# Performance work log

Measured on AMD Instinct MI355X. Metric: run time of the kernel, lower is better.

Reference implementation:

```python
import jax, jax.numpy as jnp
import numpy as np

D, S, L, W, H, V = 64, 64, 64, 300, 300, 50000
NEG = jnp.float32(-9999999.0)


def setup_inputs() -> dict:
    key = jax.random.key(0)
    ks = jax.random.split(key, 16)
    n = lambda k, shape, s=0.05: jax.random.normal(k, shape, dtype=jnp.float32) * s
    return {
        "word_indices": jax.random.randint(ks[0], (D, S, L), 0, V),
        "E": n(ks[1], (V, W), 0.1),
        "W_sent": n(ks[2], (H, W)), "b_sent": jnp.zeros((H,), jnp.float32),
        "W_par": n(ks[3], (H, H)), "b_par": jnp.zeros((H,), jnp.float32),
        "W_ch": n(ks[4], (H, H)), "b_ch": jnp.zeros((H,), jnp.float32),
        "w_root": n(ks[5], (H,)), "b_root": jnp.zeros((), jnp.float32),
        "root_embed": n(ks[6], (H,)),
        "W_r": n(ks[7], (H, 3 * H)), "b_r": jnp.zeros((H,), jnp.float32),
        "W_cls": n(ks[8], (2, H)), "b_cls": jnp.zeros((2,), jnp.float32),
    }


def reference(word_indices, E, W_sent, b_sent, W_par, b_par, W_ch, b_ch,
              w_root, b_root, root_embed, W_r, b_r, W_cls, b_cls):
    lrelu = lambda x: jax.nn.leaky_relu(x, 0.01)
    # Ragged pad+gather stage of the original, dense here (all lengths == L)
    word_embed = E[word_indices]                 # [D,S,L,W]
    # 0.5*(X[l-1] + reverse(reverse(X))[l-1]) == X[l-1]; LSTM outputs unused in source
    x_last = word_embed[:, :, -1, :]             # [D,S,W]
    enc = lrelu(x_last @ W_sent.T + b_sent)      # [D,S,H] sentence encodings
    # Pairwise parent-child edge scores (O(S^2) dots in the original loops)
    P = lrelu(enc @ W_par.T + b_par)             # [D,S,H]
    C = lrelu(enc @ W_ch.T + b_ch)               # [D,S,H]
    A = jnp.einsum('dih,djh->dij', P, C)         # [D,S,S]
    A = jnp.where(jnp.eye(S, dtype=bool)[None], NEG, A)
    A = jax.nn.softmax(A, axis=1)                # Softmax(dim=0) per doc: over parents i
    scores = enc @ w_root + b_root               # [D,S] root scores
    fri = jax.nn.softmax(scores, axis=1)         # Softmax(dim=0) over sentences
    # ri[i] = r_embeds([enc_i, sum_k A[k,i]*enc_k + fri_i*root, enc_i*sum_k A[i,k]])
    tmp = jnp.einsum('dki,dkh->dih', A, enc)     # [D,S,H]
    agg = tmp + fri[..., None] * root_embed      # [D,S,H]
    tmp3 = enc * A.sum(axis=2, keepdims=True)    # [D,S,H]
    ri = lrelu(jnp.concatenate([enc, agg, tmp3], axis=-1) @ W_r.T + b_r)  # [D,S,H]
    final = ri.mean(axis=1)                      # [D,H]
    out = final @ W_cls.T + b_cls                # [D,2]
    return out, A, fri
```

## Files before the change

### kernel.cpp

```cpp
#include <hip/hip_runtime.h>

#define NEG_INF (-9999999.0f)

typedef __attribute__((ext_vector_type(8))) short bf16x8;
typedef __attribute__((ext_vector_type(4))) float f32x4;
typedef unsigned short us;
typedef unsigned int u32;

#define MFMA16 __builtin_amdgcn_mfma_f32_16x16x32_bf16

__device__ __forceinline__ float b2f(us u) {
  union { unsigned int i; float f; } x; x.i = ((unsigned int)u) << 16; return x.f;
}
__device__ __forceinline__ us f2b(float f) {
  union { float f; unsigned int i; } x; x.f = f;
  unsigned int r = x.i + 0x7fffu + ((x.i >> 16) & 1u);
  return (us)(r >> 16);
}
__device__ __forceinline__ float lrelu(float v) { return v > 0.f ? v : 0.01f * v; }
__device__ __forceinline__ bf16x8 ld8(const us* p) { return *reinterpret_cast<const bf16x8*>(p); }
__device__ __forceinline__ int swz(int row) { return (row & 7) << 4; }

__global__ __launch_bounds__(256) void k_prep(
    const float* __restrict__ Ws, const float* __restrict__ Wp, const float* __restrict__ Wc,
    const float* __restrict__ Wr, const float* __restrict__ root,
    us* __restrict__ Wsb, us* __restrict__ Wpb, us* __restrict__ Wcb,
    us* __restrict__ Wr3b, float* __restrict__ c2) {
  int task = blockIdx.y;
  int gid = blockIdx.x * 256 + threadIdx.x;
  const int stride = 240 * 256;
  if (task < 3) {
    const float* src = (task == 0) ? Ws : (task == 1) ? Wp : Wc;
    us* dst = (task == 0) ? Wsb : (task == 1) ? Wpb : Wcb;
    for (int i = gid; i < 320 * 320; i += stride) {
      int r = i / 320, c = i - r * 320;
      dst[i] = (r < 300 && c < 300) ? f2b(src[r * 300 + c]) : (us)0;
    }
  } else if (task == 3) {
    for (int i = gid; i < 3 * 320 * 320; i += stride) {
      int seg = i / 102400, rem = i - seg * 102400;
      int r = rem / 320, c = rem - r * 320;
      Wr3b[i] = (r < 300 && c < 300) ? f2b(Wr[r * 900 + seg * 300 + c]) : (us)0;
    }
  } else {
    for (int i = gid; i < 320 * 8; i += stride) {
      int c = i >> 3, p = i & 7;
      float s = 0.f;
      if (c < 300)
        for (int h = p; h < 300; h += 8) s = fmaf(Wr[c * 900 + 300 + h], root[h], s);
      s += __shfl_xor(s, 1); s += __shfl_xor(s, 2); s += __shfl_xor(s, 4);
      if (p == 0) c2[c] = s;
    }
  }
}

template<int M, int NT, int KS>
__device__ __forceinline__ void sweepM(const us* __restrict__ Alds, const int (&rr)[M],
    int q, int lo, const us* __restrict__ Bg, int n0, f32x4 (&acc)[M][NT]) {
  const char* ab = (const char*)Alds;
  int ao[M], sw[M];
#pragma unroll
  for (int m = 0; m < M; ++m) { ao[m] = rr[m] * 640; sw[m] = swz(rr[m]); }
  const us* br[NT];
#pragma unroll
  for (int t = 0; t < NT; ++t)
    br[t] = Bg + (long)((n0 + t) * 16 + lo) * 320 + 8 * q;
  bf16x8 aC[M], aN[M], b0[NT], b1[NT];
#pragma unroll
  for (int m = 0; m < M; ++m) {
    aC[m] = *(const bf16x8*)(ab + ao[m] + ((16 * q) ^ sw[m]));
    aN[m] = *(const bf16x8*)(ab + ao[m] + ((64 + 16 * q) ^ sw[m]));
  }
#pragma unroll
  for (int t = 0; t < NT; ++t) b0[t] = ld8(br[t]);
#pragma unroll
  for (int t = 0; t < NT; ++t) b1[t] = ld8(br[t] + 32);
#pragma unroll
  for (int ks = 0; ks < KS - 2; ++ks) {
    bf16x8 aF[M], bF[NT];
    const int kb = 64 * (ks + 2) + 16 * q;
#pragma unroll
    for (int m = 0; m < M; ++m) aF[m] = *(const bf16x8*)(ab + ao[m] + (kb ^ sw[m]));
#pragma unroll
    for (int t = 0; t < NT; ++t) bF[t] = ld8(br[t] + (ks + 2) * 32);
#pragma unroll
    for (int t = 0; t < NT; ++t)
#pragma unroll
      for (int m = 0; m < M; ++m)
        acc[m][t] = MFMA16(aC[m], b0[t], acc[m][t], 0, 0, 0);
#pragma unroll
    for (int m = 0; m < M; ++m) { aC[m] = aN[m]; aN[m] = aF[m]; }
#pragma unroll
    for (int t = 0; t < NT; ++t) { b0[t] = b1[t]; b1[t] = bF[t]; }
  }
#pragma unroll
  for (int t = 0; t < NT; ++t)
#pragma unroll
    for (int m = 0; m < M; ++m) acc[m][t] = MFMA16(aC[m], b0[t], acc[m][t], 0, 0, 0);
#pragma unroll
  for (int t = 0; t < NT; ++t)
#pragma unroll
    for (int m = 0; m < M; ++m) acc[m][t] = MFMA16(aN[m], b1[t], acc[m][t], 0, 0, 0);
}

template<int NT, int KS>
__device__ __forceinline__ void sweepT(const us* __restrict__ es, int q, int lo,
    const us* __restrict__ Ag, int n0, f32x4 (&acc)[NT]) {
  const char* eb = (const char*)es;
  const int bo = lo * 640, sb = swz(lo);
  const us* ar[NT];
#pragma unroll
  for (int t = 0; t < NT; ++t)
    ar[t] = Ag + (long)((n0 + t) * 16 + lo) * 320 + 8 * q;
  bf16x8 a0[NT], a1[NT];
#pragma unroll
  for (int t = 0; t < NT; ++t) a0[t] = ld8(ar[t]);
  bf16x8 b0 = *(const bf16x8*)(eb + bo + ((16 * q) ^ sb));
#pragma unroll
  for (int t = 0; t < NT; ++t) a1[t] = ld8(ar[t] + 32);
  bf16x8 b1 = *(const bf16x8*)(eb + bo + ((64 + 16 * q) ^ sb));
#pragma unroll
  for (int ks = 0; ks < KS - 2; ++ks) {
    bf16x8 a2[NT];
#pragma unroll
    for (int t = 0; t < NT; ++t) a2[t] = ld8(ar[t] + (ks + 2) * 32);
    bf16x8 b2 = *(const bf16x8*)(eb + bo + ((64 * (ks + 2) + 16 * q) ^ sb));
#pragma unroll
    for (int t = 0; t < NT; ++t) acc[t] = MFMA16(a0[t], b0, acc[t], 0, 0, 0);
#pragma unroll
    for (int t = 0; t < NT; ++t) { a0[t] = a1[t]; a1[t] = a2[t]; }
    b0 = b1; b1 = b2;
  }
#pragma unroll
  for (int t = 0; t < NT; ++t) acc[t] = MFMA16(a0[t], b0, acc[t], 0, 0, 0);
#pragma unroll
  for (int t = 0; t < NT; ++t) acc[t] = MFMA16(a1[t], b1, acc[t], 0, 0, 0);
}

template<int NT>
__device__ __forceinline__ void sweepG(const us* __restrict__ Ab,
    const us* __restrict__ Bb, int m0, int nt0, int lo, int q, int ksn, f32x4* acc) {
  const us* ar = Ab + (long)(m0 + lo) * 320 + 8 * q;
  const us* br[NT];
#pragma unroll
  for (int t = 0; t < NT; ++t)
    br[t] = Bb + (long)((nt0 + t) * 16 + lo) * 320 + 8 * q;
  bf16x8 a0 = ld8(ar), a1 = ld8(ar + 32);
  bf16x8 b0[NT], b1[NT];
#pragma unroll
  for (int t = 0; t < NT; ++t) b0[t] = ld8(br[t]);
#pragma unroll
  for (int t = 0; t < NT; ++t) b1[t] = ld8(br[t] + 32);
  for (int ks = 0; ks < ksn - 2; ++ks) {
    bf16x8 a2 = ld8(ar + (ks + 2) * 32);
    bf16x8 b2[NT];
#pragma unroll
    for (int t = 0; t < NT; ++t) b2[t] = ld8(br[t] + (ks + 2) * 32);
#pragma unroll
    for (int t = 0; t < NT; ++t)
      acc[t] = MFMA16(a0, b0[t], acc[t], 0, 0, 0);
    a0 = a1; a1 = a2;
#pragma unroll
    for (int t = 0; t < NT; ++t) { b0[t] = b1[t]; b1[t] = b2[t]; }
  }
#pragma unroll
  for (int t = 0; t < NT; ++t)
    acc[t] = MFMA16(a0, b0[t], acc[t], 0, 0, 0);
#pragma unroll
  for (int t = 0; t < NT; ++t)
    acc[t] = MFMA16(a1, b1[t], acc[t], 0, 0, 0);
}

__global__ __launch_bounds__(256) void k_enc(
    const int* __restrict__ wi, const float* __restrict__ E,
    const us* __restrict__ Wsb, const float* __restrict__ b_sent,
    const float* __restrict__ w_root,
    us* __restrict__ encG, float* __restrict__ scG) {
  __shared__ __align__(16) us xs[16 * 320];
  __shared__ __align__(16) us es[16 * 320];
  int t = threadIdx.x;
  int r0g = blockIdx.x * 16;
  {
    int row = t >> 4, p = t & 15;
    int widx = wi[((r0g + row) << 6) + 63];
    const float4* er = (const float4*)(E + (long)widx * 300);
    char* rowb = (char*)xs + row * 640;
    int sw = swz(row);
    for (int j = p; j < 75; j += 16) {
      float4 v = er[j];
      *(ushort4*)(rowb + ((8 * j) ^ sw)) =
          make_ushort4(f2b(v.x), f2b(v.y), f2b(v.z), f2b(v.w));
    }
    for (int c = 300 + p; c < 320; c += 16)
      *(us*)(rowb + ((2 * c) ^ sw)) = 0;
  }
  __syncthreads();
  int w = t >> 6, lane = t & 63, lo = lane & 15, q = lane >> 4;
  const f32x4 z4 = {0.f, 0.f, 0.f, 0.f};
  int rr[1] = { lo };
  f32x4 acc[1][5];
#pragma unroll
  for (int b = 0; b < 5; ++b) acc[0][b] = z4;
  sweepM<1, 5, 10>(xs, rr, q, lo, Wsb, w * 5, acc);
#pragma unroll
  for (int tt = 0; tt < 5; ++tt) {
    int col = (w * 5 + tt) * 16 + lo;
    float bb = (col < 300) ? b_sent[col] : 0.f;
#pragma unroll
    for (int r = 0; r < 4; ++r) {
      int row = 4 * q + r;
      us hv = (col < 300) ? f2b(lrelu(acc[0][tt][r] + bb)) : (us)0;
      *(us*)((char*)es + row * 640 + ((2 * col) ^ swz(row))) = hv;
      encG[(long)(r0g + row) * 320 + col] = hv;
    }
  }
  __syncthreads();
  {
    int row = t >> 4, p = t & 15;
    float s = 0.f;
    for (int cch = p; cch < 38; cch += 16) {
      bf16x8 v = *(const bf16x8*)((const char*)es + row * 640 + ((16 * cch) ^ swz(row)));
#pragma unroll
      for (int e = 0; e < 8; ++e) {
        int h = cch * 8 + e;
        if (h < 300) s = fmaf(b2f((us)v[e]), w_root[h], s);
      }
    }
    s += __shfl_xor(s, 1); s += __shfl_xor(s, 2); s += __shfl_xor(s, 4); s += __shfl_xor(s, 8);
    if (p == 0) scG[r0g + row] = s;
  }
}

__global__ __launch_bounds__(256) void k_panels(
    const us* __restrict__ encG,
    const us* __restrict__ Wpb, const us* __restrict__ Wcb, const us* __restrict__ Wrb,
    const float* __restrict__ b_par, const float* __restrict__ b_ch,
    us* __restrict__ Pg, us* __restrict__ Cg, us* __restrict__ G1g, us* __restrict__ G3g,
    us* __restrict__ G2eT) {
  __shared__ __align__(16) us es[16 * 320];
  int t = threadIdx.x, task = blockIdx.y, rt = blockIdx.x;
  {
    const float4* src = (const float4*)(encG + (long)rt * 16 * 320);
    for (int i = t; i < 640; i += 256) {
      int row = i / 40, c16 = i - row * 40;
      float4 v = src[i];
      *(float4*)((char*)es + row * 640 + ((c16 * 16) ^ swz(row))) = v;
    }
  }
  __syncthreads();
  int w = t >> 6, lane = t & 63, lo = lane & 15, q = lane >> 4;
  const f32x4 z4 = {0.f, 0.f, 0.f, 0.f};
  if (task == 4) {
    f32x4 acc[5];
#pragma unroll
    for (int b = 0; b < 5; ++b) acc[b] = z4;
    sweepT<5, 10>(es, q, lo, Wrb + 102400, w * 5, acc);
#pragma unroll
    for (int tt = 0; tt < 5; ++tt)
#pragma unroll
      for (int r = 0; r < 4; ++r) {
        int h = (w * 5 + tt) * 16 + 4 * q + r;
        G2eT[(long)h * 4096 + rt * 16 + lo] = (h < 300) ? f2b(acc[tt][r]) : (us)0;
      }
  } else {
    const us* Bg = (task == 0) ? Wpb : (task == 1) ? Wcb : (task == 2) ? Wrb : Wrb + 204800;
    int rr[1] = { lo };
    f32x4 acc[1][5];
#pragma unroll
    for (int b = 0; b < 5; ++b) acc[0][b] = z4;
    sweepM<1, 5, 10>(es, rr, q, lo, Bg, w * 5, acc);
    if (task < 2) {
      const float* bias = (task == 0) ? b_par : b_ch;
      us* outb = (task == 0) ? Pg : Cg;
#pragma unroll
      for (int tt = 0; tt < 5; ++tt) {
        int col = (w * 5 + tt) * 16 + lo;
        float bb = (col < 300) ? bias[col] : 0.f;
#pragma unroll
        for (int r = 0; r < 4; ++r) {
          int row = rt * 16 + 4 * q + r;
          outb[(long)row * 320 + col] =
              (col < 300) ? f2b(lrelu(acc[0][tt][r] + bb)) : (us)0;
        }
      }
    } else {
      us* outb = (task == 2) ? G1g : G3g;
#pragma unroll
      for (int tt = 0; tt < 5; ++tt) {
        int col = (w * 5 + tt) * 16 + lo;
        if (col < 300)
#pragma unroll
          for (int r = 0; r < 4; ++r)
            outb[(long)(rt * 16 + 4 * q + r) * 320 + col] = f2b(acc[0][tt][r]);
      }
    }
  }
}

__global__ __launch_bounds__(512) void k_doc(
    const us* __restrict__ Pg, const us* __restrict__ Cg, const us* __restrict__ G2eT,
    const us* __restrict__ G1g, const us* __restrict__ G3g,
    const float* __restrict__ scG, const float* __restrict__ c2,
    const float* __restrict__ b_r, const float* __restrict__ W_cls,
    const float* __restrict__ b_cls,
    float* __restrict__ outp, float* __restrict__ outA, float* __restrict__ outF) {
  __shared__ __align__(16) float LA[64 * 68];
  __shared__ __align__(16) us AtL[64 * 72];
  __shared__ float pm[512], ps[512];
  __shared__ float friS[64], rsS[64];
  __shared__ float finP2[4 * 320];
  int d = blockIdx.x, t = threadIdx.x;
  int w = t >> 6, lane = t & 63, lo = lane & 15, q = lane >> 4;
  const f32x4 z4 = {0.f, 0.f, 0.f, 0.f};

  if (t < 64) {
    float sc = scG[d * 64 + t], m = sc;
#pragma unroll
    for (int o = 32; o > 0; o >>= 1) m = fmaxf(m, __shfl_xor(m, o));
    float e = expf(sc - m), sum = e;
#pragma unroll
    for (int o = 32; o > 0; o >>= 1) sum += __shfl_xor(sum, o);
    float f = e / sum;
    friS[t] = f;
    outF[d * 64 + t] = f;
  }

  {
    const us* Pd = Pg + (long)d * 64 * 320;
    const us* Cd = Cg + (long)d * 64 * 320;
    int m = w >> 1, np = (w & 1) * 2;
    f32x4 acc2[2] = { z4, z4 };
    sweepG<2>(Pd, Cd, m * 16, np, lo, q, 10, acc2);
#pragma unroll
    for (int r = 0; r < 4; ++r) {
      int row = m * 16 + 4 * q + r;
      int c0 = np * 16 + lo, c1 = c0 + 16;
      LA[row * 68 + c0] = (row == c0) ? NEG_INF : acc2[0][r];
      LA[row * 68 + c1] = (row == c1) ? NEG_INF : acc2[1][r];
    }
  }
  __syncthreads();

  {
    int j = lane;
    float mx = -3.0e38f;
#pragma unroll
    for (int ii = 0; ii < 8; ++ii) mx = fmaxf(mx, LA[(w * 8 + ii) * 68 + j]);
    pm[w * 64 + j] = mx;
    __syncthreads();
    float gm = pm[j];
#pragma unroll
    for (int k = 1; k < 8; ++k) gm = fmaxf(gm, pm[k * 64 + j]);
    float ev[8], ss = 0.f;
#pragma unroll
    for (int ii = 0; ii < 8; ++ii) {
      float e = expf(LA[(w * 8 + ii) * 68 + j] - gm);
      ev[ii] = e; ss += e;
    }
    ps[w * 64 + j] = ss;
    __syncthreads();
    float tot = ps[j];
#pragma unroll
    for (int k = 1; k < 8; ++k) tot += ps[k * 64 + j];
    float inv = 1.f / tot;
    float* Ad = outA + (long)d * 4096;
#pragma unroll
    for (int ii = 0; ii < 8; ++ii) {
      int i = w * 8 + ii;
      float a = ev[ii] * inv;
      Ad[i * 64 + j] = a;
      AtL[j * 72 + i] = f2b(a);
      LA[i * 68 + j] = a;
    }
  }
  __syncthreads();
  if (t < 64) {
    float s = 0.f;
    for (int jj = 0; jj < 64; ++jj) s += LA[t * 68 + jj];
    rsS[t] = s;
  }
  __syncthreads();

  {
    int mg = w & 3, nh = w >> 2;
    f32x4 a10[10];
#pragma unroll
    for (int b = 0; b < 10; ++b) a10[b] = z4;
#pragma unroll
    for (int ks = 0; ks < 2; ++ks) {
      bf16x8 aA = ld8(AtL + (mg * 16 + lo) * 72 + 32 * ks + 8 * q);
#pragma unroll
      for (int tt = 0; tt < 10; ++tt) {
        bf16x8 bv = ld8(G2eT + (long)((nh * 10 + tt) * 16 + lo) * 4096 +
                        d * 64 + 32 * ks + 8 * q);
        a10[tt] = MFMA16(aA, bv, a10[tt], 0, 0, 0);
      }
    }
#pragma unroll
    for (int tt = 0; tt < 10; ++tt) {
      int col = (nh * 10 + tt) * 16 + lo;
      if (col < 300) {
        float bb = b_r[col], cc = c2[col];
        float csum = 0.f;
#pragma unroll
        for (int r = 0; r < 4; ++r) {
          int i = mg * 16 + 4 * q + r;
          float g1 = b2f(G1g[(long)(d * 64 + i) * 320 + col]);
          float g3 = b2f(G3g[(long)(d * 64 + i) * 320 + col]);
          csum += lrelu(a10[tt][r] + g1 + rsS[i] * g3 + friS[i] * cc + bb);
        }
        csum += __shfl_xor(csum, 16);
        csum += __shfl_xor(csum, 32);
        if (q == 0) finP2[mg * 320 + col] = csum;
      }
    }
  }
  __syncthreads();

  if (t < 128) {
    int cls = t >> 6, ln = t & 63;
    float s = 0.f;
    for (int h = ln; h < 300; h += 64)
      s += (finP2[h] + finP2[320 + h] + finP2[640 + h] + finP2[960 + h]) *
           W_cls[cls * 300 + h];
#pragma unroll
    for (int o = 32; o > 0; o >>= 1) s += __shfl_xor(s, o);
    if (ln == 0) outp[d * 2 + cls] = s * 0.015625f + b_cls[cls];
  }
}

extern "C" void kernel_launch(void* const* d_in, const int* in_sizes, int n_in,
                              void* d_out, int out_size, void* d_ws, size_t ws_size,
                              hipStream_t stream) {
  const int*   wi     = (const int*)d_in[0];
  const float* E      = (const float*)d_in[1];
  const float* W_sent = (const float*)d_in[2];
  const float* b_sent = (const float*)d_in[3];
  const float* W_par  = (const float*)d_in[4];
  const float* b_par  = (const float*)d_in[5];
  const float* W_ch   = (const float*)d_in[6];
  const float* b_ch   = (const float*)d_in[7];
  const float* w_root = (const float*)d_in[8];
  const float* b_root = (const float*)d_in[9];  (void)b_root;
  const float* root_e = (const float*)d_in[10];
  const float* W_r    = (const float*)d_in[11];
  const float* b_r    = (const float*)d_in[12];
  const float* W_cls  = (const float*)d_in[13];
  const float* b_cls  = (const float*)d_in[14];

  us* B = (us*)d_ws;
  us* Wsb   = B;
  us* Wpb   = B + 102400;
  us* Wcb   = B + 204800;
  us* Wr3b  = B + 307200;
  float* c2 = (float*)(B + 614400);
  us* encG  = B + 615040;
  us* Pg    = B + 1925760;
  us* Cg    = B + 3236480;
  us* G1g   = B + 4547200;
  us* G3g   = B + 5857920;
  us* G2eT  = B + 7168640;
  float* scG = (float*)(B + 8479360);

  float* outp = (float*)d_out;
  float* outA = outp + 128;
  float* outF = outp + 128 + 262144;

  k_prep<<<dim3(240, 5), 256, 0, stream>>>(W_sent, W_par, W_ch, W_r, root_e,
                                           Wsb, Wpb, Wcb, Wr3b, c2);
  k_enc<<<256, 256, 0, stream>>>(wi, E, Wsb, b_sent, w_root, encG, scG);
  k_panels<<<dim3(256, 5), 256, 0, stream>>>(encG, Wpb, Wcb, Wr3b,
                                             b_par, b_ch, Pg, Cg, G1g, G3g, G2eT);
  k_doc<<<64, 512, 0, stream>>>(Pg, Cg, G2eT, G1g, G3g, scG, c2,
                                b_r, W_cls, b_cls, outp, outA, outF);
}
```

Measured before the change: 189.4 us.

## Overlap weight conversion with encoder and process 32-row tiles in panels

The single prep kernel is split in two. Only the W_sent conversion runs ahead of the encoder. The W_par, W_ch and W_r conversions and the root projection run as a second blockIdx.y slice of the encoder launch, so they overlap with the sentence encoding. The panel kernel now loads 32 encoded rows per block instead of 16 and computes two M-tiles per B-fragment load, which halves the global weight traffic per output row and halves the grid. This costs more registers and LDS per block, and with fewer blocks there is less parallelism.

```diff
diff --git a/kernel.cpp b/kernel.cpp
--- a/kernel.cpp
+++ b/kernel.cpp
@@ -21,164 +21,188 @@
 __device__ __forceinline__ bf16x8 ld8(const us* p) { return *reinterpret_cast<const bf16x8*>(p); }
 __device__ __forceinline__ int swz(int row) { return (row & 7) << 4; }
 
-__global__ __launch_bounds__(256) void k_prep(
-    const float* __restrict__ Ws, const float* __restrict__ Wp, const float* __restrict__ Wc,
+__global__ __launch_bounds__(256) void k_prep0(
+    const float* __restrict__ Ws, us* __restrict__ Wsb) {
+  int gid = blockIdx.x * 256 + threadIdx.x;
+  for (int i = gid; i < 320 * 320; i += 128 * 256) {
+    int r = i / 320, c = i - r * 320;
+    Wsb[i] = (r < 300 && c < 300) ? f2b(Ws[r * 300 + c]) : (us)0;
+  }
+}
+
+template<int M, int NT, int KS>
+__device__ __forceinline__ void sweepM(const us* __restrict__ Alds, const int (&rr)[M],
+    int q, int lo, const us* __restrict__ Bg, int n0, f32x4 (&acc)[M][NT]) {
+  const char* ab = (const char*)Alds;
+  int ao[M], sw[M];
+#pragma unroll
+  for (int m = 0; m < M; ++m) { ao[m] = rr[m] * 640; sw[m] = swz(rr[m]); }
+  const us* br[NT];
+#pragma unroll
+  for (int t = 0; t < NT; ++t)
+    br[t] = Bg + (long)((n0 + t) * 16 + lo) * 320 + 8 * q;
+  bf16x8 aC[M], aN[M], b0[NT], b1[NT];
+#pragma unroll
+  for (int m = 0; m < M; ++m) {
+    aC[m] = *(const bf16x8*)(ab + ao[m] + ((16 * q) ^ sw[m]));
+    aN[m] = *(const bf16x8*)(ab + ao[m] + ((64 + 16 * q) ^ sw[m]));
+  }
+#pragma unroll
+  for (int t = 0; t < NT; ++t) b0[t] = ld8(br[t]);
+#pragma unroll
+  for (int t = 0; t < NT; ++t) b1[t] = ld8(br[t] + 32);
+#pragma unroll
+  for (int ks = 0; ks < KS - 2; ++ks) {
+    bf16x8 aF[M], bF[NT];
+    const int kb = 64 * (ks + 2) + 16 * q;
+#pragma unroll
+    for (int m = 0; m < M; ++m) aF[m] = *(const bf16x8*)(ab + ao[m] + (kb ^ sw[m]));
+#pragma unroll
+    for (int t = 0; t < NT; ++t) bF[t] = ld8(br[t] + (ks + 2) * 32);
+#pragma unroll
+    for (int t = 0; t < NT; ++t)
+#pragma unroll
+      for (int m = 0; m < M; ++m)
+        acc[m][t] = MFMA16(aC[m], b0[t], acc[m][t], 0, 0, 0);
+#pragma unroll
+    for (int m = 0; m < M; ++m) { aC[m] = aN[m]; aN[m] = aF[m]; }
+#pragma unroll
+    for (int t = 0; t < NT; ++t) { b0[t] = b1[t]; b1[t] = bF[t]; }
+  }
+#pragma unroll
+  for (int t = 0; t < NT; ++t)
+#pragma unroll
+    for (int m = 0; m < M; ++m) acc[m][t] = MFMA16(aC[m], b0[t], acc[m][t], 0, 0, 0);
+#pragma unroll
+  for (int t = 0; t < NT; ++t)
+#pragma unroll
+    for (int m = 0; m < M; ++m) acc[m][t] = MFMA16(aN[m], b1[t], acc[m][t], 0, 0, 0);
+}
+
+template<int NT, int KS>
+__device__ __forceinline__ void sweepT2(const us* __restrict__ es, int q, int lo,
+    const us* __restrict__ Ag, int n0, f32x4 (&acc)[2][NT]) {
+  const char* eb = (const char*)es;
+  int bo[2] = { lo * 640, (lo + 16) * 640 };
+  int sb[2] = { swz(lo), swz(lo + 16) };
+  const us* ar[NT];
+#pragma unroll
+  for (int t = 0; t < NT; ++t)
+    ar[t] = Ag + (long)((n0 + t) * 16 + lo) * 320 + 8 * q;
+  bf16x8 a0[NT], a1[NT], bC[2], bN[2];
+#pragma unroll
+  for (int t = 0; t < NT; ++t) a0[t] = ld8(ar[t]);
+#pragma unroll
+  for (int h = 0; h < 2; ++h)
+    bC[h] = *(const bf16x8*)(eb + bo[h] + ((16 * q) ^ sb[h]));
+#pragma unroll
+  for (int t = 0; t < NT; ++t) a1[t] = ld8(ar[t] + 32);
+#pragma unroll
+  for (int h = 0; h < 2; ++h)
+    bN[h] = *(const bf16x8*)(eb + bo[h] + ((64 + 16 * q) ^ sb[h]));
+#pragma unroll
+  for (int ks = 0; ks < KS - 2; ++ks) {
+    bf16x8 a2[NT], bF[2];
+    const int kb = 64 * (ks + 2) + 16 * q;
+#pragma unroll
+    for (int t = 0; t < NT; ++t) a2[t] = ld8(ar[t] + (ks + 2) * 32);
+#pragma unroll
+    for (int h = 0; h < 2; ++h)
+      bF[h] = *(const bf16x8*)(eb + bo[h] + (kb ^ sb[h]));
+#pragma unroll
+    for (int t = 0; t < NT; ++t) {
+      acc[0][t] = MFMA16(a0[t], bC[0], acc[0][t], 0, 0, 0);
+      acc[1][t] = MFMA16(a0[t], bC[1], acc[1][t], 0, 0, 0);
+    }
+#pragma unroll
+    for (int t = 0; t < NT; ++t) { a0[t] = a1[t]; a1[t] = a2[t]; }
+#pragma unroll
+    for (int h = 0; h < 2; ++h) { bC[h] = bN[h]; bN[h] = bF[h]; }
+  }
+#pragma unroll
+  for (int t = 0; t < NT; ++t) {
+    acc[0][t] = MFMA16(a0[t], bC[0], acc[0][t], 0, 0, 0);
+    acc[1][t] = MFMA16(a0[t], bC[1], acc[1][t], 0, 0, 0);
+  }
+#pragma unroll
+  for (int t = 0; t < NT; ++t) {
+    acc[0][t] = MFMA16(a1[t], bN[0], acc[0][t], 0, 0, 0);
+    acc[1][t] = MFMA16(a1[t], bN[1], acc[1][t], 0, 0, 0);
+  }
+}
+
+template<int NT>
+__device__ __forceinline__ void sweepG(const us* __restrict__ Ab,
+    const us* __restrict__ Bb, int m0, int nt0, int lo, int q, int ksn, f32x4* acc) {
+  const us* ar = Ab + (long)(m0 + lo) * 320 + 8 * q;
+  const us* br[NT];
+#pragma unroll
+  for (int t = 0; t < NT; ++t)
+    br[t] = Bb + (long)((nt0 + t) * 16 + lo) * 320 + 8 * q;
+  bf16x8 a0 = ld8(ar), a1 = ld8(ar + 32);
+  bf16x8 b0[NT], b1[NT];
+#pragma unroll
+  for (int t = 0; t < NT; ++t) b0[t] = ld8(br[t]);
+#pragma unroll
+  for (int t = 0; t < NT; ++t) b1[t] = ld8(br[t] + 32);
+  for (int ks = 0; ks < ksn - 2; ++ks) {
+    bf16x8 a2 = ld8(ar + (ks + 2) * 32);
+    bf16x8 b2[NT];
+#pragma unroll
+    for (int t = 0; t < NT; ++t) b2[t] = ld8(br[t] + (ks + 2) * 32);
+#pragma unroll
+    for (int t = 0; t < NT; ++t)
+      acc[t] = MFMA16(a0, b0[t], acc[t], 0, 0, 0);
+    a0 = a1; a1 = a2;
+#pragma unroll
+    for (int t = 0; t < NT; ++t) { b0[t] = b1[t]; b1[t] = b2[t]; }
+  }
+#pragma unroll
+  for (int t = 0; t < NT; ++t)
+    acc[t] = MFMA16(a0, b0[t], acc[t], 0, 0, 0);
+#pragma unroll
+  for (int t = 0; t < NT; ++t)
+    acc[t] = MFMA16(a1, b1[t], acc[t], 0, 0, 0);
+}
+
+__global__ __launch_bounds__(256) void k_encprep(
+    const int* __restrict__ wi, const float* __restrict__ E,
+    const us* __restrict__ Wsb, const float* __restrict__ b_sent,
+    const float* __restrict__ w_root,
+    const float* __restrict__ Wp, const float* __restrict__ Wc,
     const float* __restrict__ Wr, const float* __restrict__ root,
-    us* __restrict__ Wsb, us* __restrict__ Wpb, us* __restrict__ Wcb,
-    us* __restrict__ Wr3b, float* __restrict__ c2) {
-  int task = blockIdx.y;
-  int gid = blockIdx.x * 256 + threadIdx.x;
-  const int stride = 240 * 256;
-  if (task < 3) {
-    const float* src = (task == 0) ? Ws : (task == 1) ? Wp : Wc;
-    us* dst = (task == 0) ? Wsb : (task == 1) ? Wpb : Wcb;
-    for (int i = gid; i < 320 * 320; i += stride) {
-      int r = i / 320, c = i - r * 320;
-      dst[i] = (r < 300 && c < 300) ? f2b(src[r * 300 + c]) : (us)0;
-    }
-  } else if (task == 3) {
-    for (int i = gid; i < 3 * 320 * 320; i += stride) {
-      int seg = i / 102400, rem = i - seg * 102400;
+    us* __restrict__ encG, float* __restrict__ scG,
+    us* __restrict__ Wpb, us* __restrict__ Wcb, us* __restrict__ Wr3b,
+    float* __restrict__ c2) {
+  int t = threadIdx.x;
+  if (blockIdx.y == 1) {
+    int gid = blockIdx.x * 256 + t;
+    const int stride = 256 * 256;
+    for (int i = gid; i < 5 * 102400; i += stride) {
+      int p = i / 102400, rem = i - p * 102400;
       int r = rem / 320, c = rem - r * 320;
-      Wr3b[i] = (r < 300 && c < 300) ? f2b(Wr[r * 900 + seg * 300 + c]) : (us)0;
-    }
-  } else {
-    for (int i = gid; i < 320 * 8; i += stride) {
-      int c = i >> 3, p = i & 7;
+      us v = 0;
+      if (r < 300 && c < 300) {
+        if (p == 0)      v = f2b(Wp[r * 300 + c]);
+        else if (p == 1) v = f2b(Wc[r * 300 + c]);
+        else             v = f2b(Wr[r * 900 + (p - 2) * 300 + c]);
+      }
+      if (p == 0)      Wpb[rem] = v;
+      else if (p == 1) Wcb[rem] = v;
+      else             Wr3b[(p - 2) * 102400 + rem] = v;
+    }
+    if (gid < 2560) {
+      int c = gid >> 3, p = gid & 7;
       float s = 0.f;
       if (c < 300)
         for (int h = p; h < 300; h += 8) s = fmaf(Wr[c * 900 + 300 + h], root[h], s);
       s += __shfl_xor(s, 1); s += __shfl_xor(s, 2); s += __shfl_xor(s, 4);
       if (p == 0) c2[c] = s;
     }
-  }
-}
-
-template<int M, int NT, int KS>
-__device__ __forceinline__ void sweepM(const us* __restrict__ Alds, const int (&rr)[M],
-    int q, int lo, const us* __restrict__ Bg, int n0, f32x4 (&acc)[M][NT]) {
-  const char* ab = (const char*)Alds;
-  int ao[M], sw[M];
-#pragma unroll
-  for (int m = 0; m < M; ++m) { ao[m] = rr[m] * 640; sw[m] = swz(rr[m]); }
-  const us* br[NT];
-#pragma unroll
-  for (int t = 0; t < NT; ++t)
-    br[t] = Bg + (long)((n0 + t) * 16 + lo) * 320 + 8 * q;
-  bf16x8 aC[M], aN[M], b0[NT], b1[NT];
-#pragma unroll
-  for (int m = 0; m < M; ++m) {
-    aC[m] = *(const bf16x8*)(ab + ao[m] + ((16 * q) ^ sw[m]));
-    aN[m] = *(const bf16x8*)(ab + ao[m] + ((64 + 16 * q) ^ sw[m]));
-  }
-#pragma unroll
-  for (int t = 0; t < NT; ++t) b0[t] = ld8(br[t]);
-#pragma unroll
-  for (int t = 0; t < NT; ++t) b1[t] = ld8(br[t] + 32);
-#pragma unroll
-  for (int ks = 0; ks < KS - 2; ++ks) {
-    bf16x8 aF[M], bF[NT];
-    const int kb = 64 * (ks + 2) + 16 * q;
-#pragma unroll
-    for (int m = 0; m < M; ++m) aF[m] = *(const bf16x8*)(ab + ao[m] + (kb ^ sw[m]));
-#pragma unroll
-    for (int t = 0; t < NT; ++t) bF[t] = ld8(br[t] + (ks + 2) * 32);
-#pragma unroll
-    for (int t = 0; t < NT; ++t)
-#pragma unroll
-      for (int m = 0; m < M; ++m)
-        acc[m][t] = MFMA16(aC[m], b0[t], acc[m][t], 0, 0, 0);
-#pragma unroll
-    for (int m = 0; m < M; ++m) { aC[m] = aN[m]; aN[m] = aF[m]; }
-#pragma unroll
-    for (int t = 0; t < NT; ++t) { b0[t] = b1[t]; b1[t] = bF[t]; }
-  }
-#pragma unroll
-  for (int t = 0; t < NT; ++t)
-#pragma unroll
-    for (int m = 0; m < M; ++m) acc[m][t] = MFMA16(aC[m], b0[t], acc[m][t], 0, 0, 0);
-#pragma unroll
-  for (int t = 0; t < NT; ++t)
-#pragma unroll
-    for (int m = 0; m < M; ++m) acc[m][t] = MFMA16(aN[m], b1[t], acc[m][t], 0, 0, 0);
-}
-
-template<int NT, int KS>
-__device__ __forceinline__ void sweepT(const us* __restrict__ es, int q, int lo,
-    const us* __restrict__ Ag, int n0, f32x4 (&acc)[NT]) {
-  const char* eb = (const char*)es;
-  const int bo = lo * 640, sb = swz(lo);
-  const us* ar[NT];
-#pragma unroll
-  for (int t = 0; t < NT; ++t)
-    ar[t] = Ag + (long)((n0 + t) * 16 + lo) * 320 + 8 * q;
-  bf16x8 a0[NT], a1[NT];
-#pragma unroll
-  for (int t = 0; t < NT; ++t) a0[t] = ld8(ar[t]);
-  bf16x8 b0 = *(const bf16x8*)(eb + bo + ((16 * q) ^ sb));
-#pragma unroll
-  for (int t = 0; t < NT; ++t) a1[t] = ld8(ar[t] + 32);
-  bf16x8 b1 = *(const bf16x8*)(eb + bo + ((64 + 16 * q) ^ sb));
-#pragma unroll
-  for (int ks = 0; ks < KS - 2; ++ks) {
-    bf16x8 a2[NT];
-#pragma unroll
-    for (int t = 0; t < NT; ++t) a2[t] = ld8(ar[t] + (ks + 2) * 32);
-    bf16x8 b2 = *(const bf16x8*)(eb + bo + ((64 * (ks + 2) + 16 * q) ^ sb));
-#pragma unroll
-    for (int t = 0; t < NT; ++t) acc[t] = MFMA16(a0[t], b0, acc[t], 0, 0, 0);
-#pragma unroll
-    for (int t = 0; t < NT; ++t) { a0[t] = a1[t]; a1[t] = a2[t]; }
-    b0 = b1; b1 = b2;
-  }
-#pragma unroll
-  for (int t = 0; t < NT; ++t) acc[t] = MFMA16(a0[t], b0, acc[t], 0, 0, 0);
-#pragma unroll
-  for (int t = 0; t < NT; ++t) acc[t] = MFMA16(a1[t], b1, acc[t], 0, 0, 0);
-}
-
-template<int NT>
-__device__ __forceinline__ void sweepG(const us* __restrict__ Ab,
-    const us* __restrict__ Bb, int m0, int nt0, int lo, int q, int ksn, f32x4* acc) {
-  const us* ar = Ab + (long)(m0 + lo) * 320 + 8 * q;
-  const us* br[NT];
-#pragma unroll
-  for (int t = 0; t < NT; ++t)
-    br[t] = Bb + (long)((nt0 + t) * 16 + lo) * 320 + 8 * q;
-  bf16x8 a0 = ld8(ar), a1 = ld8(ar + 32);
-  bf16x8 b0[NT], b1[NT];
-#pragma unroll
-  for (int t = 0; t < NT; ++t) b0[t] = ld8(br[t]);
-#pragma unroll
-  for (int t = 0; t < NT; ++t) b1[t] = ld8(br[t] + 32);
-  for (int ks = 0; ks < ksn - 2; ++ks) {
-    bf16x8 a2 = ld8(ar + (ks + 2) * 32);
-    bf16x8 b2[NT];
-#pragma unroll
-    for (int t = 0; t < NT; ++t) b2[t] = ld8(br[t] + (ks + 2) * 32);
-#pragma unroll
-    for (int t = 0; t < NT; ++t)
-      acc[t] = MFMA16(a0, b0[t], acc[t], 0, 0, 0);
-    a0 = a1; a1 = a2;
-#pragma unroll
-    for (int t = 0; t < NT; ++t) { b0[t] = b1[t]; b1[t] = b2[t]; }
-  }
-#pragma unroll
-  for (int t = 0; t < NT; ++t)
-    acc[t] = MFMA16(a0, b0[t], acc[t], 0, 0, 0);
-#pragma unroll
-  for (int t = 0; t < NT; ++t)
-    acc[t] = MFMA16(a1, b1[t], acc[t], 0, 0, 0);
-}
-
-__global__ __launch_bounds__(256) void k_enc(
-    const int* __restrict__ wi, const float* __restrict__ E,
-    const us* __restrict__ Wsb, const float* __restrict__ b_sent,
-    const float* __restrict__ w_root,
-    us* __restrict__ encG, float* __restrict__ scG) {
+    return;
+  }
   __shared__ __align__(16) us xs[16 * 320];
   __shared__ __align__(16) us es[16 * 320];
-  int t = threadIdx.x;
   int r0g = blockIdx.x * 16;
   {
     int row = t >> 4, p = t & 15;
@@ -237,11 +261,11 @@
     const float* __restrict__ b_par, const float* __restrict__ b_ch,
     us* __restrict__ Pg, us* __restrict__ Cg, us* __restrict__ G1g, us* __restrict__ G3g,
     us* __restrict__ G2eT) {
-  __shared__ __align__(16) us es[16 * 320];
+  __shared__ __align__(16) us es[32 * 320];
   int t = threadIdx.x, task = blockIdx.y, rt = blockIdx.x;
   {
-    const float4* src = (const float4*)(encG + (long)rt * 16 * 320);
-    for (int i = t; i < 640; i += 256) {
+    const float4* src = (const float4*)(encG + (long)rt * 32 * 320);
+    for (int i = t; i < 1280; i += 256) {
       int row = i / 40, c16 = i - row * 40;
       float4 v = src[i];
       *(float4*)((char*)es + row * 640 + ((c16 * 16) ^ swz(row))) = v;
@@ -251,48 +275,59 @@
   int w = t >> 6, lane = t & 63, lo = lane & 15, q = lane >> 4;
   const f32x4 z4 = {0.f, 0.f, 0.f, 0.f};
   if (task == 4) {
-    f32x4 acc[5];
-#pragma unroll
-    for (int b = 0; b < 5; ++b) acc[b] = z4;
-    sweepT<5, 10>(es, q, lo, Wrb + 102400, w * 5, acc);
-#pragma unroll
-    for (int tt = 0; tt < 5; ++tt)
-#pragma unroll
-      for (int r = 0; r < 4; ++r) {
-        int h = (w * 5 + tt) * 16 + 4 * q + r;
-        G2eT[(long)h * 4096 + rt * 16 + lo] = (h < 300) ? f2b(acc[tt][r]) : (us)0;
-      }
+    f32x4 acc[2][5];
+#pragma unroll
+    for (int a = 0; a < 2; ++a)
+#pragma unroll
+      for (int b = 0; b < 5; ++b) acc[a][b] = z4;
+    sweepT2<5, 10>(es, q, lo, Wrb + 102400, w * 5, acc);
+#pragma unroll
+    for (int half = 0; half < 2; ++half)
+#pragma unroll
+      for (int tt = 0; tt < 5; ++tt)
+#pragma unroll
+        for (int r = 0; r < 4; ++r) {
+          int h = (w * 5 + tt) * 16 + 4 * q + r;
+          G2eT[(long)h * 4096 + rt * 32 + half * 16 + lo] =
+              (h < 300) ? f2b(acc[half][tt][r]) : (us)0;
+        }
   } else {
     const us* Bg = (task == 0) ? Wpb : (task == 1) ? Wcb : (task == 2) ? Wrb : Wrb + 204800;
-    int rr[1] = { lo };
-    f32x4 acc[1][5];
-#pragma unroll
-    for (int b = 0; b < 5; ++b) acc[0][b] = z4;
-    sweepM<1, 5, 10>(es, rr, q, lo, Bg, w * 5, acc);
+    int rr[2] = { lo, 16 + lo };
+    f32x4 acc[2][5];
+#pragma unroll
+    for (int a = 0; a < 2; ++a)
+#pragma unroll
+      for (int b = 0; b < 5; ++b) acc[a][b] = z4;
+    sweepM<2, 5, 10>(es, rr, q, lo, Bg, w * 5, acc);
     if (task < 2) {
       const float* bias = (task == 0) ? b_par : b_ch;
       us* outb = (task == 0) ? Pg : Cg;
 #pragma unroll
-      for (int tt = 0; tt < 5; ++tt) {
-        int col = (w * 5 + tt) * 16 + lo;
-        float bb = (col < 300) ? bias[col] : 0.f;
-#pragma unroll
-        for (int r = 0; r < 4; ++r) {
-          int row = rt * 16 + 4 * q + r;
-          outb[(long)row * 320 + col] =
-              (col < 300) ? f2b(lrelu(acc[0][tt][r] + bb)) : (us)0;
+      for (int m = 0; m < 2; ++m)
+#pragma unroll
+        for (int tt = 0; tt < 5; ++tt) {
+          int col = (w * 5 + tt) * 16 + lo;
+          float bb = (col < 300) ? bias[col] : 0.f;
+#pragma unroll
+          for (int r = 0; r < 4; ++r) {
+            int row = rt * 32 + m * 16 + 4 * q + r;
+            outb[(long)row * 320 + col] =
+                (col < 300) ? f2b(lrelu(acc[m][tt][r] + bb)) : (us)0;
+          }
         }
-      }
     } else {
       us* outb = (task == 2) ? G1g : G3g;
 #pragma unroll
-      for (int tt = 0; tt < 5; ++tt) {
-        int col = (w * 5 + tt) * 16 + lo;
-        if (col < 300)
-#pragma unroll
-          for (int r = 0; r < 4; ++r)
-            outb[(long)(rt * 16 + 4 * q + r) * 320 + col] = f2b(acc[0][tt][r]);
-      }
+      for (int m = 0; m < 2; ++m)
+#pragma unroll
+        for (int tt = 0; tt < 5; ++tt) {
+          int col = (w * 5 + tt) * 16 + lo;
+          if (col < 300)
+#pragma unroll
+            for (int r = 0; r < 4; ++r)
+              outb[(long)(rt * 32 + m * 16 + 4 * q + r) * 320 + col] = f2b(acc[m][tt][r]);
+        }
     }
   }
 }
@@ -466,10 +501,11 @@
   float* outA = outp + 128;
   float* outF = outp + 128 + 262144;
 
-  k_prep<<<dim3(240, 5), 256, 0, stream>>>(W_sent, W_par, W_ch, W_r, root_e,
-                                           Wsb, Wpb, Wcb, Wr3b, c2);
-  k_enc<<<256, 256, 0, stream>>>(wi, E, Wsb, b_sent, w_root, encG, scG);
-  k_panels<<<dim3(256, 5), 256, 0, stream>>>(encG, Wpb, Wcb, Wr3b,
+  k_prep0<<<128, 256, 0, stream>>>(W_sent, Wsb);
+  k_encprep<<<dim3(256, 2), 256, 0, stream>>>(wi, E, Wsb, b_sent, w_root,
+                                              W_par, W_ch, W_r, root_e,
+                                              encG, scG, Wpb, Wcb, Wr3b, c2);
+  k_panels<<<dim3(128, 5), 256, 0, stream>>>(encG, Wpb, Wcb, Wr3b,
                                              b_par, b_ch, Pg, Cg, G1g, G3g, G2eT);
   k_doc<<<64, 512, 0, stream>>>(Pg, Cg, G2eT, G1g, G3g, scG, c2,
                                 b_r, W_cls, b_cls, outp, outA, outF);
```

New measurement: 174.1 us. 1.09x faster.
